# Kernel tuning notes

Measured on AMD Instinct MI355X. Metric: run time of the kernel, lower is better.

## Reference

```python
import jax, jax.numpy as jnp
import numpy as np

LEAK = 0.95
THRESHOLD = 1.0
CLAMP = 3.0
LN_EPS = 1e-5


def setup_inputs() -> dict:
    key = jax.random.key(0)
    k1, k2 = jax.random.split(key)
    B, S, V, D = 8, 2048, 57344, 1536
    token_ids = jax.random.randint(k1, (B, S), 0, V, dtype=jnp.int64)
    emb_table = jax.random.normal(k2, (V, D), dtype=jnp.float32) * 0.02
    gamma = jnp.ones((D,), dtype=jnp.float32)
    beta = jnp.zeros((D,), dtype=jnp.float32)
    return {"token_ids": token_ids, "emb_table": emb_table, "gamma": gamma, "beta": beta}


def _layernorm(x, gamma, beta):
    mu = jnp.mean(x, axis=-1, keepdims=True)
    var = jnp.mean(jnp.square(x - mu), axis=-1, keepdims=True)
    return (x - mu) * jax.lax.rsqrt(var + LN_EPS) * gamma + beta


def _lif_scan(x):
    # x: [B, S, D]; sequential LIF recurrence over time axis S
    B, S, D = x.shape
    v0 = jnp.zeros((B, D), dtype=x.dtype)

    def step(v, xt):
        v = v * LEAK + xt
        v = jnp.clip(v, -CLAMP, CLAMP)
        spike = (v >= THRESHOLD).astype(x.dtype)
        return v * (1.0 - spike), spike

    _, spikes = jax.lax.scan(step, v0, jnp.swapaxes(x, 0, 1))  # spikes: [S, B, D]
    return jnp.swapaxes(spikes, 0, 1)


def reference(token_ids, emb_table, gamma, beta):
    x = emb_table[token_ids]          # [B, S, D] embedding lookup
    x = _layernorm(x, gamma, beta)    # continuous residual stream
    spikes = _lif_scan(x)             # 0/1 spike tensor [B, S, D]
    return spikes, x
```

## Files before the change

kernel.cpp:

```cpp
#include <hip/hip_runtime.h>


constexpr int Bv = 8, Sv = 2048, Dv = 1536;
constexpr int Cn = 32;
constexpr int Ln = Sv / Cn;
constexpr int Wn = 64;
constexpr int BD = Bv * Dv;
constexpr int TNMAX = Ln + Wn;

constexpr size_t FLAG_OFF  = 0;
constexpr size_t STATS_OFF = 64;
constexpr size_t SE_OFF    = STATS_OFF + (size_t)2 * Bv * Sv * 8;
constexpr size_t WS_NEED   = SE_OFF + (size_t)Cn * BD * 16;

__device__ __forceinline__ double ln_x64(float e, double mu, double rs,
                                         double gd, double bd) {
#pragma clang fp contract(off)
    return (((double)e - mu) * rs) * gd + bd;
}
__device__ __forceinline__ double lif_step(double v, double x, bool& spike) {
#pragma clang fp contract(off)
    double vv = v * 0.95;
    vv = vv + x;
    vv = fmin(fmax(vv, -3.0), 3.0);
    spike = (vv >= 1.0);
    return spike ? 0.0 : vv;
}

extern "C" __global__ __launch_bounds__(1024)
void detect_tok64(const int* __restrict__ tok, int* __restrict__ flag)
{
    __shared__ int any_nz;
    if (threadIdx.x == 0) any_nz = 0;
    __syncthreads();
    int nz = 0;
    for (int i = threadIdx.x; i < (Bv * Sv) / 2; i += 1024) nz |= tok[2 * i + 1];
    if (nz) atomicOr(&any_nz, 1);
    __syncthreads();
    if (threadIdx.x == 0) flag[0] = (any_nz == 0) ? 1 : 0;
}

extern "C" __global__ __launch_bounds__(128)
void ln_stats_kernel(const int* __restrict__ tok,
                     const float* __restrict__ emb,
                     double* __restrict__ stats,
                     const int* __restrict__ tok64_flag)
{
#pragma clang fp contract(off)
    __shared__ double p1[2], p2[2];

    const int row = blockIdx.x;
    const int t   = threadIdx.x;
    const int lane = t & 63, wave = t >> 6;

    const int shift = tok64_flag[0];
    const long long tk = (long long)tok[(size_t)row << shift];
    const float* src = emb + tk * (long long)Dv;

    float4 xv[3];
#pragma unroll
    for (int k = 0; k < 3; ++k) xv[k] = reinterpret_cast<const float4*>(src)[t + 128 * k];

    double s = 0.0;
#pragma unroll
    for (int k = 0; k < 3; ++k) {
        s += (double)xv[k].x; s += (double)xv[k].y;
        s += (double)xv[k].z; s += (double)xv[k].w;
    }
#pragma unroll
    for (int off = 1; off < 64; off <<= 1) s += __shfl_xor(s, off);
    if (lane == 0) p1[wave] = s;
    __syncthreads();
    const double mu = (p1[0] + p1[1]) / 1536.0;

    double q = 0.0;
#pragma unroll
    for (int k = 0; k < 3; ++k) {
        double d0 = (double)xv[k].x - mu; q += d0 * d0;
        double d1 = (double)xv[k].y - mu; q += d1 * d1;
        double d2 = (double)xv[k].z - mu; q += d2 * d2;
        double d3 = (double)xv[k].w - mu; q += d3 * d3;
    }
#pragma unroll
    for (int off = 1; off < 64; off <<= 1) q += __shfl_xor(q, off);
    if (lane == 0) p2[wave] = q;
    __syncthreads();
    const double var  = (p2[0] + p2[1]) / 1536.0;
    const double rstd = 1.0 / sqrt(var + 1e-5);

    if (t == 0) { stats[2 * row] = mu; stats[2 * row + 1] = rstd; }
}

extern "C" __global__ __launch_bounds__(256)
void lif64_spec(const int* __restrict__ tok,
                const float* __restrict__ emb,
                const float* __restrict__ gamma,
                const float* __restrict__ beta,
                const double* __restrict__ stats,
                float* __restrict__ x_out,
                float* __restrict__ spk,
                double2* __restrict__ se,
                const int* __restrict__ tok64_flag)
{
    constexpr int DBLK = Dv / 256;
    __shared__ int     tokl[TNMAX];
    __shared__ double2 statl[TNMAX];

    const int t    = threadIdx.x;
    const int bid  = blockIdx.x;
    const int dblk = bid % DBLK;
    const int c    = (bid / DBLK) % Cn;
    const int b    = bid / (DBLK * Cn);
    const int d    = dblk * 256 + t;

    const int s0 = c * Ln;
    const int sw = (c == 0) ? 0 : s0 - Wn;
    const int TN = s0 + Ln - sw;
    const int warm = s0 - sw;
    const int rowbase = b * Sv;

    if (t < TN) {
        const int row = rowbase + sw + t;
        const int shift = tok64_flag[0];
        tokl[t]  = tok[(size_t)row << shift];
        statl[t] = reinterpret_cast<const double2*>(stats)[row];
    }
    __syncthreads();

    const double gd = (double)gamma[d];
    const double bd = (double)beta[d];
    float* sp = spk   + (size_t)b * Sv * Dv + d;
    float* xo = x_out + (size_t)b * Sv * Dv + d;

    constexpr int U = 8;
    float ecur[U], enxt[U];
#pragma unroll
    for (int k = 0; k < U; ++k)
        ecur[k] = emb[(long long)tokl[k] * Dv + d];

    double v = 0.0, vstart = 0.0;
    for (int i = 0; i < TN; i += U) {
        if (i + U < TN) {
#pragma unroll
            for (int k = 0; k < U; ++k)
                enxt[k] = emb[(long long)tokl[i + U + k] * Dv + d];
        }
#pragma unroll
        for (int k = 0; k < U; ++k) {
            const int idx = i + k;
            if (idx == warm) vstart = v;
            const double2 st = statl[idx];
            const double x = ln_x64(ecur[k], st.x, st.y, gd, bd);
            bool spike;
            const double vn = lif_step(v, x, spike);
            if (idx >= warm) {
                const size_t off = (size_t)(sw + idx) * Dv;
                __builtin_nontemporal_store((float)x, &xo[off]);
                __builtin_nontemporal_store(spike ? 1.0f : 0.0f, &sp[off]);
            }
            v = vn;
        }
#pragma unroll
        for (int k = 0; k < U; ++k) ecur[k] = enxt[k];
    }

    const size_t chain = (size_t)b * Dv + d;
    double2 a; a.x = vstart; a.y = v;
    se[(size_t)c * BD + chain] = a;
}

extern "C" __global__ __launch_bounds__(64)
void lif64_fixup(const int* __restrict__ tok,
                 const float* __restrict__ emb,
                 const float* __restrict__ gamma,
                 const float* __restrict__ beta,
                 const double* __restrict__ stats,
                 const double2* __restrict__ se,
                 float* __restrict__ spk,
                 const int* __restrict__ tok64_flag)
{
    const int gid = blockIdx.x * 64 + threadIdx.x;
    const int b = gid / Dv;
    const int d = gid - b * Dv;
    const int shift = tok64_flag[0];
    const double gd = (double)gamma[d];
    const double bd = (double)beta[d];
    const int rowbase = b * Sv;
    float* sp = spk + (size_t)b * Sv * Dv + d;

    double2 buf[4], nbuf[4];
#pragma unroll
    for (int j = 0; j < 4; ++j) buf[j] = se[(size_t)j * BD + gid];

    double v = 0.0;
    for (int c4 = 0; c4 < Cn; c4 += 4) {
        if (c4 + 4 < Cn) {
#pragma unroll
            for (int j = 0; j < 4; ++j)
                nbuf[j] = se[(size_t)(c4 + 4 + j) * BD + gid];
        }
#pragma unroll
        for (int j = 0; j < 4; ++j) {
            const int c = c4 + j;
            if (v == buf[j].x) { v = buf[j].y; continue; }
            constexpr int U = 8;
            const int s0 = c * Ln;
            float  ecur[U], enxt[U];
            double mcur[U], mnxt[U], rcur[U], rnxt[U];
#pragma unroll
            for (int k = 0; k < U; ++k) {
                const int row = rowbase + s0 + k;
                const long long tk = (long long)tok[(size_t)row << shift];
                ecur[k] = emb[tk * (long long)Dv + d];
                mcur[k] = stats[2 * row];
                rcur[k] = stats[2 * row + 1];
            }
            for (int i = 0; i < Ln; i += U) {
                if (i + U < Ln) {
#pragma unroll
                    for (int k = 0; k < U; ++k) {
                        const int row = rowbase + s0 + i + U + k;
                        const long long tk = (long long)tok[(size_t)row << shift];
                        enxt[k] = emb[tk * (long long)Dv + d];
                        mnxt[k] = stats[2 * row];
                        rnxt[k] = stats[2 * row + 1];
                    }
                }
#pragma unroll
                for (int k = 0; k < U; ++k) {
                    const double x = ln_x64(ecur[k], mcur[k], rcur[k], gd, bd);
                    bool spike;
                    v = lif_step(v, x, spike);
                    sp[(size_t)(s0 + i + k) * Dv] = spike ? 1.0f : 0.0f;
                }
#pragma unroll
                for (int k = 0; k < U; ++k) {
                    ecur[k] = enxt[k]; mcur[k] = mnxt[k]; rcur[k] = rnxt[k];
                }
            }
        }
#pragma unroll
        for (int j = 0; j < 4; ++j) buf[j] = nbuf[j];
    }
}

extern "C" __global__ __launch_bounds__(64)
void lif64_seq(const int* __restrict__ tok,
               const float* __restrict__ emb,
               const float* __restrict__ gamma,
               const float* __restrict__ beta,
               const double* __restrict__ stats,
               float* __restrict__ x_out,
               float* __restrict__ spk,
               const int* __restrict__ flags)
{
    const int gid = blockIdx.x * 64 + threadIdx.x;
    const int b = gid / Dv;
    const int d = gid - b * Dv;
    const int shift = flags[0];
    const int rowbase = b * Sv;
    const double gd = (double)gamma[d];
    const double bd = (double)beta[d];
    float* sp = spk   + (size_t)b * Sv * Dv + d;
    float* xo = x_out + (size_t)b * Sv * Dv + d;

    constexpr int U = 8;
    float  ecur[U], enxt[U];
    double mcur[U], mnxt[U], rcur[U], rnxt[U];
#pragma unroll
    for (int k = 0; k < U; ++k) {
        const int row = rowbase + k;
        const long long tk = (long long)tok[(size_t)row << shift];
        ecur[k] = emb[tk * (long long)Dv + d];
        mcur[k] = stats[2 * row];
        rcur[k] = stats[2 * row + 1];
    }
    double v = 0.0;
    for (int s = 0; s < Sv; s += U) {
        if (s + U < Sv) {
#pragma unroll
            for (int k = 0; k < U; ++k) {
                const int row = rowbase + s + U + k;
                const long long tk = (long long)tok[(size_t)row << shift];
                enxt[k] = emb[tk * (long long)Dv + d];
                mnxt[k] = stats[2 * row];
                rnxt[k] = stats[2 * row + 1];
            }
        }
#pragma unroll
        for (int k = 0; k < U; ++k) {
            const double x = ln_x64(ecur[k], mcur[k], rcur[k], gd, bd);
            bool spike;
            v = lif_step(v, x, spike);
            const size_t off = (size_t)(s + k) * Dv;
            __builtin_nontemporal_store((float)x, &xo[off]);
            __builtin_nontemporal_store(spike ? 1.0f : 0.0f, &sp[off]);
        }
#pragma unroll
        for (int k = 0; k < U; ++k) { ecur[k] = enxt[k]; mcur[k] = mnxt[k]; rcur[k] = rnxt[k]; }
    }
}

extern "C" void kernel_launch(void* const* d_in, const int* in_sizes, int n_in,
                              void* d_out, int out_size, void* d_ws, size_t ws_size,
                              hipStream_t stream)
{
    const int*   tok   = (const int*)  d_in[0];
    const float* emb   = (const float*)d_in[1];
    const float* gamma = (const float*)d_in[2];
    const float* beta  = (const float*)d_in[3];

    float* out = (float*)d_out;
    float* spk = out;
    float* x   = out + (size_t)Bv * Sv * Dv;

    int*    flg   = (int*)((char*)d_ws + FLAG_OFF);
    double* stats = (double*)((char*)d_ws + STATS_OFF);

    detect_tok64<<<1, 1024, 0, stream>>>(tok, flg);
    ln_stats_kernel<<<Bv * Sv, 128, 0, stream>>>(tok, emb, stats, flg);

    if (ws_size >= WS_NEED) {
        double2* se = (double2*)((char*)d_ws + SE_OFF);
        lif64_spec<<<Bv * Cn * (Dv / 256), 256, 0, stream>>>(
            tok, emb, gamma, beta, stats, x, spk, se, flg);
        lif64_fixup<<<BD / 64, 64, 0, stream>>>(
            tok, emb, gamma, beta, stats, se, spk, flg);
    } else {
        lif64_seq<<<BD / 64, 64, 0, stream>>>(
            tok, emb, gamma, beta, stats, x, spk, flg);
    }
}
```

Baseline: 133.6 us.

## Write layernorm output from stats kernel with float4 stores; LIF kernels emit spikes only

The stats kernel already holds each embedding row in registers, so it now also applies gamma/beta and writes the normalized x row with coalesced float4 stores. The LIF scan kernels no longer write x with strided per-column scalar stores, which halves their store traffic. The speculative LIF kernel also raises its unroll from 8 to 16 and adds an occupancy hint to launch_bounds. The risk is higher register pressure, which could cause spills or lower occupancy.

Measured after the change: 135.7 us. About the same (+1.6%).

```diff
diff --git a/kernel.cpp b/kernel.cpp
--- a/kernel.cpp
+++ b/kernel.cpp
@@ -43,6 +43,9 @@
 extern "C" __global__ __launch_bounds__(128)
 void ln_stats_kernel(const int* __restrict__ tok,
                      const float* __restrict__ emb,
+                     const float* __restrict__ gamma,
+                     const float* __restrict__ beta,
+                     float* __restrict__ x_out,
                      double* __restrict__ stats,
                      const int* __restrict__ tok64_flag)
 {
@@ -89,15 +92,28 @@
     const double rstd = 1.0 / sqrt(var + 1e-5);
 
     if (t == 0) { stats[2 * row] = mu; stats[2 * row + 1] = rstd; }
-}
-
-extern "C" __global__ __launch_bounds__(256)
+
+    float* dst = x_out + (long long)row * Dv;
+#pragma unroll
+    for (int k = 0; k < 3; ++k) {
+        const int f4 = t + 128 * k;
+        const float4 g4 = reinterpret_cast<const float4*>(gamma)[f4];
+        const float4 b4 = reinterpret_cast<const float4*>(beta)[f4];
+        float4 o;
+        o.x = (float)((((double)xv[k].x - mu) * rstd) * (double)g4.x + (double)b4.x);
+        o.y = (float)((((double)xv[k].y - mu) * rstd) * (double)g4.y + (double)b4.y);
+        o.z = (float)((((double)xv[k].z - mu) * rstd) * (double)g4.z + (double)b4.z);
+        o.w = (float)((((double)xv[k].w - mu) * rstd) * (double)g4.w + (double)b4.w);
+        reinterpret_cast<float4*>(dst)[f4] = o;
+    }
+}
+
+extern "C" __global__ __launch_bounds__(256, 6)
 void lif64_spec(const int* __restrict__ tok,
                 const float* __restrict__ emb,
                 const float* __restrict__ gamma,
                 const float* __restrict__ beta,
                 const double* __restrict__ stats,
-                float* __restrict__ x_out,
                 float* __restrict__ spk,
                 double2* __restrict__ se,
                 const int* __restrict__ tok64_flag)
@@ -129,10 +145,9 @@
 
     const double gd = (double)gamma[d];
     const double bd = (double)beta[d];
-    float* sp = spk   + (size_t)b * Sv * Dv + d;
-    float* xo = x_out + (size_t)b * Sv * Dv + d;
-
-    constexpr int U = 8;
+    float* sp = spk + (size_t)b * Sv * Dv + d;
+
+    constexpr int U = 16;
     float ecur[U], enxt[U];
 #pragma unroll
     for (int k = 0; k < U; ++k)
@@ -153,11 +168,9 @@
             const double x = ln_x64(ecur[k], st.x, st.y, gd, bd);
             bool spike;
             const double vn = lif_step(v, x, spike);
-            if (idx >= warm) {
-                const size_t off = (size_t)(sw + idx) * Dv;
-                __builtin_nontemporal_store((float)x, &xo[off]);
-                __builtin_nontemporal_store(spike ? 1.0f : 0.0f, &sp[off]);
-            }
+            if (idx >= warm)
+                __builtin_nontemporal_store(spike ? 1.0f : 0.0f,
+                                            &sp[(size_t)(sw + idx) * Dv]);
             v = vn;
         }
 #pragma unroll
@@ -250,7 +263,6 @@
                const float* __restrict__ gamma,
                const float* __restrict__ beta,
                const double* __restrict__ stats,
-               float* __restrict__ x_out,
                float* __restrict__ spk,
                const int* __restrict__ flags)
 {
@@ -261,8 +273,7 @@
     const int rowbase = b * Sv;
     const double gd = (double)gamma[d];
     const double bd = (double)beta[d];
-    float* sp = spk   + (size_t)b * Sv * Dv + d;
-    float* xo = x_out + (size_t)b * Sv * Dv + d;
+    float* sp = spk + (size_t)b * Sv * Dv + d;
 
     constexpr int U = 8;
     float  ecur[U], enxt[U];
@@ -292,9 +303,7 @@
             const double x = ln_x64(ecur[k], mcur[k], rcur[k], gd, bd);
             bool spike;
             v = lif_step(v, x, spike);
-            const size_t off = (size_t)(s + k) * Dv;
-            __builtin_nontemporal_store((float)x, &xo[off]);
-            __builtin_nontemporal_store(spike ? 1.0f : 0.0f, &sp[off]);
+            __builtin_nontemporal_store(spike ? 1.0f : 0.0f, &sp[(size_t)(s + k) * Dv]);
         }
 #pragma unroll
         for (int k = 0; k < U; ++k) { ecur[k] = enxt[k]; mcur[k] = mnxt[k]; rcur[k] = rnxt[k]; }
@@ -318,16 +327,15 @@
     double* stats = (double*)((char*)d_ws + STATS_OFF);
 
     detect_tok64<<<1, 1024, 0, stream>>>(tok, flg);
-    ln_stats_kernel<<<Bv * Sv, 128, 0, stream>>>(tok, emb, stats, flg);
+    ln_stats_kernel<<<Bv * Sv, 128, 0, stream>>>(tok, emb, gamma, beta, x, stats, flg);
 
     if (ws_size >= WS_NEED) {
         double2* se = (double2*)((char*)d_ws + SE_OFF);
         lif64_spec<<<Bv * Cn * (Dv / 256), 256, 0, stream>>>(
-            tok, emb, gamma, beta, stats, x, spk, se, flg);
+            tok, emb, gamma, beta, stats, spk, se, flg);
         lif64_fixup<<<BD / 64, 64, 0, stream>>>(
             tok, emb, gamma, beta, stats, se, spk, flg);
     } else {
-        lif64_seq<<<BD / 64, 64, 0, stream>>>(
-            tok, emb, gamma, beta, stats, x, spk, flg);
-    }
-}
+        lif64_seq<<<BD / 64, 64, 0, stream>>>(tok, emb, gamma, beta, stats, spk, flg);
+    }
+}
```
